# Kernel tuning notes

Measured on AMD Instinct MI355X. Metric: run time of the kernel, lower is better.

The kernel has to match this reference:

```python
import jax, jax.numpy as jnp
import numpy as np

DIM = 512
HEADS = 8
DIM_HEAD = 64
INNER = HEADS * DIM_HEAD  # 512
EPS = 1e-5


def _per_head_layernorm(t, gamma, beta):
    # t: [b, h, n, k]; gamma/beta: [h, k] (distinct LayerNorm per head)
    mu = jnp.mean(t, axis=-1, keepdims=True)
    var = jnp.mean(jnp.square(t - mu), axis=-1, keepdims=True)
    t_hat = (t - mu) * jax.lax.rsqrt(var + EPS)
    return t_hat * gamma[None, :, None, :] + beta[None, :, None, :]


def setup_inputs() -> dict:
    key = jax.random.key(0)
    ks = jax.random.split(key, 6)
    x = jax.random.normal(ks[0], (4, 8192, DIM), dtype=jnp.float32)
    # xavier_normal_ with gain=1e-4 on to_qkv weight [3*inner, dim]
    std_qkv = 1e-4 * np.sqrt(2.0 / (3 * INNER + DIM))
    W_qkv = jax.random.normal(ks[1], (3 * INNER, DIM), dtype=jnp.float32) * std_qkv
    gamma_K = jnp.ones((HEADS, DIM_HEAD), dtype=jnp.float32)
    beta_K = jnp.zeros((HEADS, DIM_HEAD), dtype=jnp.float32)
    gamma_V = jnp.ones((HEADS, DIM_HEAD), dtype=jnp.float32)
    beta_V = jnp.zeros((HEADS, DIM_HEAD), dtype=jnp.float32)
    std_out = np.sqrt(1.0 / INNER)
    W_out = jax.random.uniform(ks[2], (DIM, INNER), dtype=jnp.float32, minval=-std_out, maxval=std_out)
    b_out = jax.random.uniform(ks[3], (DIM,), dtype=jnp.float32, minval=-std_out, maxval=std_out)
    return {"x": x, "W_qkv": W_qkv, "gamma_K": gamma_K, "beta_K": beta_K,
            "gamma_V": gamma_V, "beta_V": beta_V, "W_out": W_out, "b_out": b_out}


def reference(x, W_qkv, gamma_K, beta_K, gamma_V, beta_V, W_out, b_out):
    b, n, _ = x.shape
    qkv = jnp.einsum('bnd,ed->bne', x, W_qkv)  # [b, n, 3*inner]
    q, k, v = jnp.split(qkv, 3, axis=-1)

    def to_heads(t):  # [b, n, h*k] -> [b, h, n, k]
        return t.reshape(b, n, HEADS, DIM_HEAD).transpose(0, 2, 1, 3)

    q, k, v = to_heads(q), to_heads(k), to_heads(v)
    k = _per_head_layernorm(k, gamma_K, beta_K)
    v = _per_head_layernorm(v, gamma_V, beta_V)

    # Galerkin linear attention: (K^T V)/n then Q @ (.)  -> O(n * d^2)
    p_attn = jnp.einsum('bhnk,bhnv->bhkv', k, v) / n  # [b, h, k, k]
    out = jnp.einsum('bhnk,bhkv->bhnv', q, p_attn)    # [b, h, n, k]
    out = out.transpose(0, 2, 1, 3).reshape(b, n, INNER)
    return jnp.einsum('bne,de->bnd', out, W_out) + b_out
```

## Files before the change

### kernel.cpp

```cpp
#include <hip/hip_runtime.h>


typedef __attribute__((ext_vector_type(8))) short bf16x8;
typedef __attribute__((ext_vector_type(4))) float f32x4;
typedef __attribute__((ext_vector_type(4))) unsigned short u16x4;

__device__ __forceinline__ unsigned short f2bf(float f) {
  unsigned int u = __builtin_bit_cast(unsigned int, f);
  u += 0x7FFFu + ((u >> 16) & 1u);
  return (unsigned short)(u >> 16);
}

__device__ __forceinline__ f32x4 mfma16(bf16x8 a, bf16x8 b, f32x4 c) {
  return __builtin_amdgcn_mfma_f32_16x16x32_bf16(a, b, c, 0, 0, 0);
}

__device__ __forceinline__ void gload16(const void* g, void* l) {
  __builtin_amdgcn_global_load_lds(
      (const __attribute__((address_space(1))) void*)g,
      (__attribute__((address_space(3))) void*)l, 16, 0, 0);
}

__global__ void k_cvt_bf16(const float* __restrict__ src,
                           unsigned short* __restrict__ dst, int n4) {
  int i = blockIdx.x * blockDim.x + threadIdx.x;
  if (i < n4) {
    float4 v = ((const float4*)src)[i];
    u16x4 o;
    o[0] = f2bf(v.x); o[1] = f2bf(v.y); o[2] = f2bf(v.z); o[3] = f2bf(v.w);
    ((u16x4*)dst)[i] = o;
  }
}

__device__ __forceinline__ void stage_tile(const unsigned short* pa,
                                           const unsigned short* pb,
                                           unsigned short* As, unsigned short* Bs,
                                           int w) {
#pragma unroll
  for (int j = 0; j < 4; ++j) {
    gload16(pa + j * 8 * 512, As + w * 2048 + j * 512);
    gload16(pb + j * 8 * 512, Bs + w * 2048 + j * 512);
  }
}

__device__ __forceinline__ void compute_tile(const unsigned short* As,
                                             const unsigned short* Bs,
                                             int wr, int wc, int g, int c16,
                                             f32x4 acc[4][4]) {
#pragma unroll
  for (int ks = 0; ks < 2; ++ks) {
    const int kcol = (ks * 32 + g * 8) ^ ((c16 & 7) << 3);
    bf16x8 af[4], bfv[4];
#pragma unroll
    for (int mi = 0; mi < 4; ++mi)
      af[mi] = *(const bf16x8*)&As[(wr * 64 + mi * 16 + c16) * 64 + kcol];
#pragma unroll
    for (int ni = 0; ni < 4; ++ni)
      bfv[ni] = *(const bf16x8*)&Bs[(wc * 64 + ni * 16 + c16) * 64 + kcol];
#pragma unroll
    for (int mi = 0; mi < 4; ++mi)
#pragma unroll
      for (int ni = 0; ni < 4; ++ni)
        acc[mi][ni] = mfma16(af[mi], bfv[ni], acc[mi][ni]);
  }
}

__launch_bounds__(256)
__global__ void k1_kvp(const unsigned short* __restrict__ xb,
                       const unsigned short* __restrict__ wqkvb,
                       const float* __restrict__ gK, const float* __restrict__ bK,
                       const float* __restrict__ gV, const float* __restrict__ bV,
                       float* __restrict__ P) {
  __shared__ __align__(16) unsigned short As[2][8192];
  __shared__ __align__(16) unsigned short Bs[2][8192];
  const int rt = blockIdx.x, h = blockIdx.y;
  const int tid = (int)threadIdx.x;
  const int l = tid & 63, w = tid >> 6;
  const int wr = w >> 1, wc = w & 1;
  const int g = l >> 4, c16 = l & 15;
  const int row0 = rt * 128;
  const int swz = ((l & 7) ^ (l >> 3)) * 8;

  const unsigned short* gsA = xb + (row0 + w * 32 + (l >> 3)) * 512 + swz;
  const int bcol = (w < 2) ? (512 + h * 64 + w * 32) : (1024 + h * 64 + (w - 2) * 32);
  const unsigned short* gsB = wqkvb + (bcol + (l >> 3)) * 512 + swz;

  f32x4 acc[4][4] = {};
  stage_tile(gsA, gsB, As[0], Bs[0], w);
  __syncthreads();
  for (int kt = 0; kt < 7; ++kt) {
    stage_tile(gsA + (kt + 1) * 64, gsB + (kt + 1) * 64,
               As[(kt + 1) & 1], Bs[(kt + 1) & 1], w);
    compute_tile(As[kt & 1], Bs[kt & 1], wr, wc, g, c16, acc);
    __syncthreads();
  }
  compute_tile(As[1], Bs[1], wr, wc, g, c16, acc);

  const float* gamma = (wc == 0) ? gK : gV;
  const float* beta  = (wc == 0) ? bK : bV;
  float gm[4], bt[4];
#pragma unroll
  for (int ni = 0; ni < 4; ++ni) {
    gm[ni] = gamma[h * 64 + ni * 16 + c16];
    bt[ni] = beta[h * 64 + ni * 16 + c16];
  }

  unsigned short* Kl = &As[0][0];
  unsigned short* Vl = &Bs[0][0];
  unsigned short* dst = (wc == 0) ? Kl : Vl;

#pragma unroll
  for (int mi = 0; mi < 4; ++mi) {
    float mean4[4], rs4[4];
#pragma unroll
    for (int r = 0; r < 4; ++r) {
      float a0 = acc[mi][0][r], a1 = acc[mi][1][r];
      float a2 = acc[mi][2][r], a3 = acc[mi][3][r];
      float s1 = a0 + a1 + a2 + a3;
      float s2 = a0 * a0 + a1 * a1 + a2 * a2 + a3 * a3;
#pragma unroll
      for (int m = 1; m <= 8; m <<= 1) {
        s1 += __shfl_xor(s1, m, 64);
        s2 += __shfl_xor(s2, m, 64);
      }
      const float mean = s1 * (1.0f / 64.0f);
      const float var = s2 * (1.0f / 64.0f) - mean * mean;
      mean4[r] = mean;
      rs4[r] = rsqrtf(var + 1e-5f);
    }
    const int n0 = wr * 64 + mi * 16 + g * 4;
#pragma unroll
    for (int ni = 0; ni < 4; ++ni) {
      const int d = ni * 16 + c16;
      u16x4 o;
#pragma unroll
      for (int r = 0; r < 4; ++r)
        o[r] = f2bf((acc[mi][ni][r] - mean4[r]) * rs4[r] * gm[ni] + bt[ni]);
      *(u16x4*)&dst[d * 128 + (((n0 >> 3) ^ c16) << 3) + (n0 & 7)] = o;
    }
  }
  __syncthreads();

  f32x4 pacc[4] = {};
#pragma unroll
  for (int ks = 0; ks < 4; ++ks) {
    const int p8 = (ks * 4 + g);
    bf16x8 af = *(const bf16x8*)&Kl[(w * 16 + c16) * 128 + ((p8 ^ c16) << 3)];
#pragma unroll
    for (int ni = 0; ni < 4; ++ni) {
      bf16x8 bfv = *(const bf16x8*)&Vl[(ni * 16 + c16) * 128 + ((p8 ^ c16) << 3)];
      pacc[ni] = mfma16(af, bfv, pacc[ni]);
    }
  }
  const int bh = (row0 >> 13) * 8 + h;
  float* Pp = P + bh * 4096;
#pragma unroll
  for (int ni = 0; ni < 4; ++ni)
#pragma unroll
    for (int r = 0; r < 4; ++r)
      atomicAdd(&Pp[(w * 16 + g * 4 + r) * 64 + ni * 16 + c16], pacc[ni][r]);
}

__launch_bounds__(256)
__global__ void k3a_g(const float* __restrict__ Wqkv,
                      const float* __restrict__ P,
                      unsigned short* __restrict__ Gt) {
  __shared__ float Pl[64 * 64];
  const int bh = blockIdx.x, dd = blockIdx.y;
  const int b = bh >> 3, h = bh & 7;
  const int t = (int)threadIdx.x;
  for (int i = t; i < 1024; i += 256)
    ((float4*)Pl)[i] = ((const float4*)(P + bh * 4096))[i];
  __syncthreads();

  const int qg = t >> 6, dl = t & 63;
  const int d = dd * 64 + dl;
  float acc[16] = {};
  for (int dh = 0; dh < 64; ++dh) {
    const float wq = Wqkv[(h * 64 + dh) * 512 + d];
    const float* pr = &Pl[dh * 64 + qg * 16];
#pragma unroll
    for (int i = 0; i < 16; ++i) acc[i] += pr[i] * wq;
  }
  unsigned short* go = &Gt[(b * 512 + d) * 512 + h * 64 + qg * 16];
#pragma unroll
  for (int i = 0; i < 16; ++i) go[i] = f2bf(acc[i] * (1.0f / 8192.0f));
}

__launch_bounds__(256)
__global__ void k3b_m(const unsigned short* __restrict__ wob,
                      const unsigned short* __restrict__ Gt,
                      unsigned short* __restrict__ Mb) {
  __shared__ __align__(16) unsigned short As[2][8192];
  __shared__ __align__(16) unsigned short Bs[2][8192];
  const int rt = blockIdx.x, ct = blockIdx.y, b = blockIdx.z;
  const int tid = (int)threadIdx.x;
  const int l = tid & 63, w = tid >> 6;
  const int wr = w >> 1, wc = w & 1;
  const int g = l >> 4, c16 = l & 15;
  const int row0 = rt * 128, col0 = ct * 128;
  const int swz = ((l & 7) ^ (l >> 3)) * 8;

  const unsigned short* gsA = wob + (row0 + w * 32 + (l >> 3)) * 512 + swz;
  const unsigned short* gsB = Gt + b * 262144 + (col0 + w * 32 + (l >> 3)) * 512 + swz;

  f32x4 acc[4][4] = {};
  stage_tile(gsA, gsB, As[0], Bs[0], w);
  __syncthreads();
  for (int kt = 0; kt < 7; ++kt) {
    stage_tile(gsA + (kt + 1) * 64, gsB + (kt + 1) * 64,
               As[(kt + 1) & 1], Bs[(kt + 1) & 1], w);
    compute_tile(As[kt & 1], Bs[kt & 1], wr, wc, g, c16, acc);
    __syncthreads();
  }
  compute_tile(As[1], Bs[1], wr, wc, g, c16, acc);

#pragma unroll
  for (int mi = 0; mi < 4; ++mi)
#pragma unroll
    for (int ni = 0; ni < 4; ++ni) {
      const int colg = col0 + wc * 64 + ni * 16 + c16;
#pragma unroll
      for (int r = 0; r < 4; ++r) {
        const int rowg = row0 + wr * 64 + mi * 16 + g * 4 + r;
        Mb[(b * 512 + rowg) * 512 + colg] = f2bf(acc[mi][ni][r]);
      }
    }
}

__launch_bounds__(256)
__global__ void k4_final(const unsigned short* __restrict__ xb,
                         const unsigned short* __restrict__ Mb,
                         const float* __restrict__ bout,
                         float* __restrict__ y) {
  __shared__ __align__(16) unsigned short As[2][8192];
  __shared__ __align__(16) unsigned short Bs[2][8192];
  const int rt = blockIdx.x, ct = blockIdx.y;
  const int tid = (int)threadIdx.x;
  const int l = tid & 63, w = tid >> 6;
  const int wr = w >> 1, wc = w & 1;
  const int g = l >> 4, c16 = l & 15;
  const int row0 = rt * 128, col0 = ct * 128;
  const int bb = row0 >> 13;
  const int swz = ((l & 7) ^ (l >> 3)) * 8;

  const unsigned short* gsA = xb + (row0 + w * 32 + (l >> 3)) * 512 + swz;
  const unsigned short* gsB = Mb + bb * 262144 + (col0 + w * 32 + (l >> 3)) * 512 + swz;

  f32x4 acc[4][4] = {};
  stage_tile(gsA, gsB, As[0], Bs[0], w);
  __syncthreads();
  for (int kt = 0; kt < 7; ++kt) {
    stage_tile(gsA + (kt + 1) * 64, gsB + (kt + 1) * 64,
               As[(kt + 1) & 1], Bs[(kt + 1) & 1], w);
    compute_tile(As[kt & 1], Bs[kt & 1], wr, wc, g, c16, acc);
    __syncthreads();
  }
  compute_tile(As[1], Bs[1], wr, wc, g, c16, acc);

  float bo[4];
#pragma unroll
  for (int ni = 0; ni < 4; ++ni)
    bo[ni] = bout[col0 + wc * 64 + ni * 16 + c16];
#pragma unroll
  for (int mi = 0; mi < 4; ++mi)
#pragma unroll
    for (int ni = 0; ni < 4; ++ni) {
      const int colg = col0 + wc * 64 + ni * 16 + c16;
#pragma unroll
      for (int r = 0; r < 4; ++r) {
        const int rowg = row0 + wr * 64 + mi * 16 + g * 4 + r;
        y[rowg * 512 + colg] = acc[mi][ni][r] + bo[ni];
      }
    }
}

extern "C" void kernel_launch(void* const* d_in, const int* in_sizes, int n_in,
                              void* d_out, int out_size, void* d_ws, size_t ws_size,
                              hipStream_t stream) {
  (void)in_sizes; (void)n_in; (void)out_size; (void)ws_size;
  const float* x    = (const float*)d_in[0];
  const float* Wqkv = (const float*)d_in[1];
  const float* gK   = (const float*)d_in[2];
  const float* bK   = (const float*)d_in[3];
  const float* gV   = (const float*)d_in[4];
  const float* bV   = (const float*)d_in[5];
  const float* Wout = (const float*)d_in[6];
  const float* bout = (const float*)d_in[7];
  float* y = (float*)d_out;

  char* w = (char*)d_ws;
  unsigned short* xb  = (unsigned short*)(w);
  unsigned short* Wb  = (unsigned short*)(w + 33554432);
  unsigned short* Wob = (unsigned short*)(w + 35127296);
  float*          P   = (float*)         (w + 35651584);
  unsigned short* Gt  = (unsigned short*)(w + 36175872);
  unsigned short* Mb  = (unsigned short*)(w + 38273024);

  k_cvt_bf16<<<16384, 256, 0, stream>>>(x, xb, 4194304);
  k_cvt_bf16<<<768, 256, 0, stream>>>(Wqkv, Wb, 196608);
  k_cvt_bf16<<<256, 256, 0, stream>>>(Wout, Wob, 65536);
  hipMemsetAsync(P, 0, 524288, stream);

  k1_kvp<<<dim3(256, 8), 256, 0, stream>>>(xb, Wb, gK, bK, gV, bV, P);
  k3a_g<<<dim3(32, 8), 256, 0, stream>>>(Wqkv, P, Gt);
  k3b_m<<<dim3(4, 4, 4), 256, 0, stream>>>(Wob, Gt, Mb);
  k4_final<<<dim3(256, 4), 256, 0, stream>>>(xb, Mb, bout, y);
}
```

Before: 145.9 us.

## Replace atomics with partial-sum buffer, single-buffer LDS, remap blocks across XCDs

The K/V-projection kernel now writes per-row-tile partial K^T V products to a workspace buffer, and a new reduction kernel sums them. This replaces the fp32 atomicAdd accumulation and the memset. All three GEMM kernels drop LDS double-buffering for a single buffer with two barriers per k-step. This halves LDS use, which may raise occupancy, but it loses the overlap between loads and compute. k1 and k4 also remap block IDs so neighbouring tiles land on the same XCD, aiming for better L2 locality. The cost is an extra 32 MB partial-buffer write and read plus one more kernel launch.

```diff
diff --git a/kernel.cpp b/kernel.cpp
--- a/kernel.cpp
+++ b/kernel.cpp
@@ -70,10 +70,12 @@
                        const unsigned short* __restrict__ wqkvb,
                        const float* __restrict__ gK, const float* __restrict__ bK,
                        const float* __restrict__ gV, const float* __restrict__ bV,
-                       float* __restrict__ P) {
-  __shared__ __align__(16) unsigned short As[2][8192];
-  __shared__ __align__(16) unsigned short Bs[2][8192];
-  const int rt = blockIdx.x, h = blockIdx.y;
+                       float* __restrict__ Ppart) {
+  __shared__ __align__(16) unsigned short As[8192];
+  __shared__ __align__(16) unsigned short Bs[8192];
+  const int bid = (int)blockIdx.x;
+  const int wgid = (bid & 7) * 256 + (bid >> 3);
+  const int rt = wgid >> 3, h = wgid & 7;
   const int tid = (int)threadIdx.x;
   const int l = tid & 63, w = tid >> 6;
   const int wr = w >> 1, wc = w & 1;
@@ -86,15 +88,12 @@
   const unsigned short* gsB = wqkvb + (bcol + (l >> 3)) * 512 + swz;
 
   f32x4 acc[4][4] = {};
-  stage_tile(gsA, gsB, As[0], Bs[0], w);
-  __syncthreads();
-  for (int kt = 0; kt < 7; ++kt) {
-    stage_tile(gsA + (kt + 1) * 64, gsB + (kt + 1) * 64,
-               As[(kt + 1) & 1], Bs[(kt + 1) & 1], w);
-    compute_tile(As[kt & 1], Bs[kt & 1], wr, wc, g, c16, acc);
-    __syncthreads();
-  }
-  compute_tile(As[1], Bs[1], wr, wc, g, c16, acc);
+  for (int kt = 0; kt < 8; ++kt) {
+    stage_tile(gsA + kt * 64, gsB + kt * 64, As, Bs, w);
+    __syncthreads();
+    compute_tile(As, Bs, wr, wc, g, c16, acc);
+    __syncthreads();
+  }
 
   const float* gamma = (wc == 0) ? gK : gV;
   const float* beta  = (wc == 0) ? bK : bV;
@@ -105,10 +104,7 @@
     bt[ni] = beta[h * 64 + ni * 16 + c16];
   }
 
-  unsigned short* Kl = &As[0][0];
-  unsigned short* Vl = &Bs[0][0];
-  unsigned short* dst = (wc == 0) ? Kl : Vl;
-
+  unsigned short* dst = (wc == 0) ? As : Bs;
 #pragma unroll
   for (int mi = 0; mi < 4; ++mi) {
     float mean4[4], rs4[4];
@@ -131,12 +127,11 @@
     const int n0 = wr * 64 + mi * 16 + g * 4;
 #pragma unroll
     for (int ni = 0; ni < 4; ++ni) {
-      const int d = ni * 16 + c16;
       u16x4 o;
 #pragma unroll
       for (int r = 0; r < 4; ++r)
         o[r] = f2bf((acc[mi][ni][r] - mean4[r]) * rs4[r] * gm[ni] + bt[ni]);
-      *(u16x4*)&dst[d * 128 + (((n0 >> 3) ^ c16) << 3) + (n0 & 7)] = o;
+      *(u16x4*)&dst[(ni * 16 + c16) * 128 + (((n0 >> 3) ^ c16) << 3) + (n0 & 7)] = o;
     }
   }
   __syncthreads();
@@ -144,21 +139,33 @@
   f32x4 pacc[4] = {};
 #pragma unroll
   for (int ks = 0; ks < 4; ++ks) {
-    const int p8 = (ks * 4 + g);
-    bf16x8 af = *(const bf16x8*)&Kl[(w * 16 + c16) * 128 + ((p8 ^ c16) << 3)];
+    const int grp = ((ks * 4 + g) ^ c16) << 3;
+    bf16x8 af = *(const bf16x8*)&As[(w * 16 + c16) * 128 + grp];
 #pragma unroll
     for (int ni = 0; ni < 4; ++ni) {
-      bf16x8 bfv = *(const bf16x8*)&Vl[(ni * 16 + c16) * 128 + ((p8 ^ c16) << 3)];
-      pacc[ni] = mfma16(af, bfv, pacc[ni]);
-    }
-  }
-  const int bh = (row0 >> 13) * 8 + h;
-  float* Pp = P + bh * 4096;
+      bf16x8 bv = *(const bf16x8*)&Bs[(ni * 16 + c16) * 128 + grp];
+      pacc[ni] = mfma16(af, bv, pacc[ni]);
+    }
+  }
+  const int bh = (rt >> 6) * 8 + h;
+  float* Pp = Ppart + ((size_t)(bh * 64 + (rt & 63))) * 4096;
 #pragma unroll
   for (int ni = 0; ni < 4; ++ni)
 #pragma unroll
     for (int r = 0; r < 4; ++r)
-      atomicAdd(&Pp[(w * 16 + g * 4 + r) * 64 + ni * 16 + c16], pacc[ni][r]);
+      Pp[(w * 16 + g * 4 + r) * 64 + ni * 16 + c16] = pacc[ni][r];
+}
+
+__launch_bounds__(256)
+__global__ void k_preduce(const float* __restrict__ Ppart,
+                          float* __restrict__ P) {
+  const int bh = blockIdx.x;
+  const int e = blockIdx.y * 256 + threadIdx.x;
+  const float* src = Ppart + (size_t)bh * 64 * 4096 + e;
+  float s = 0.f;
+#pragma unroll 8
+  for (int sl = 0; sl < 64; ++sl) s += src[sl * 4096];
+  P[bh * 4096 + e] = s;
 }
 
 __launch_bounds__(256)
@@ -191,8 +198,8 @@
 __global__ void k3b_m(const unsigned short* __restrict__ wob,
                       const unsigned short* __restrict__ Gt,
                       unsigned short* __restrict__ Mb) {
-  __shared__ __align__(16) unsigned short As[2][8192];
-  __shared__ __align__(16) unsigned short Bs[2][8192];
+  __shared__ __align__(16) unsigned short As[8192];
+  __shared__ __align__(16) unsigned short Bs[8192];
   const int rt = blockIdx.x, ct = blockIdx.y, b = blockIdx.z;
   const int tid = (int)threadIdx.x;
   const int l = tid & 63, w = tid >> 6;
@@ -205,15 +212,12 @@
   const unsigned short* gsB = Gt + b * 262144 + (col0 + w * 32 + (l >> 3)) * 512 + swz;
 
   f32x4 acc[4][4] = {};
-  stage_tile(gsA, gsB, As[0], Bs[0], w);
-  __syncthreads();
-  for (int kt = 0; kt < 7; ++kt) {
-    stage_tile(gsA + (kt + 1) * 64, gsB + (kt + 1) * 64,
-               As[(kt + 1) & 1], Bs[(kt + 1) & 1], w);
-    compute_tile(As[kt & 1], Bs[kt & 1], wr, wc, g, c16, acc);
-    __syncthreads();
-  }
-  compute_tile(As[1], Bs[1], wr, wc, g, c16, acc);
+  for (int kt = 0; kt < 8; ++kt) {
+    stage_tile(gsA + kt * 64, gsB + kt * 64, As, Bs, w);
+    __syncthreads();
+    compute_tile(As, Bs, wr, wc, g, c16, acc);
+    __syncthreads();
+  }
 
 #pragma unroll
   for (int mi = 0; mi < 4; ++mi)
@@ -233,9 +237,11 @@
                          const unsigned short* __restrict__ Mb,
                          const float* __restrict__ bout,
                          float* __restrict__ y) {
-  __shared__ __align__(16) unsigned short As[2][8192];
-  __shared__ __align__(16) unsigned short Bs[2][8192];
-  const int rt = blockIdx.x, ct = blockIdx.y;
+  __shared__ __align__(16) unsigned short As[8192];
+  __shared__ __align__(16) unsigned short Bs[8192];
+  const int bid = (int)blockIdx.x;
+  const int wgid = (bid & 7) * 128 + (bid >> 3);
+  const int rt = wgid >> 2, ct = wgid & 3;
   const int tid = (int)threadIdx.x;
   const int l = tid & 63, w = tid >> 6;
   const int wr = w >> 1, wc = w & 1;
@@ -248,15 +254,12 @@
   const unsigned short* gsB = Mb + bb * 262144 + (col0 + w * 32 + (l >> 3)) * 512 + swz;
 
   f32x4 acc[4][4] = {};
-  stage_tile(gsA, gsB, As[0], Bs[0], w);
-  __syncthreads();
-  for (int kt = 0; kt < 7; ++kt) {
-    stage_tile(gsA + (kt + 1) * 64, gsB + (kt + 1) * 64,
-               As[(kt + 1) & 1], Bs[(kt + 1) & 1], w);
-    compute_tile(As[kt & 1], Bs[kt & 1], wr, wc, g, c16, acc);
-    __syncthreads();
-  }
-  compute_tile(As[1], Bs[1], wr, wc, g, c16, acc);
+  for (int kt = 0; kt < 8; ++kt) {
+    stage_tile(gsA + kt * 64, gsB + kt * 64, As, Bs, w);
+    __syncthreads();
+    compute_tile(As, Bs, wr, wc, g, c16, acc);
+    __syncthreads();
+  }
 
   float bo[4];
 #pragma unroll
@@ -290,20 +293,21 @@
   float* y = (float*)d_out;
 
   char* w = (char*)d_ws;
-  unsigned short* xb  = (unsigned short*)(w);
-  unsigned short* Wb  = (unsigned short*)(w + 33554432);
-  unsigned short* Wob = (unsigned short*)(w + 35127296);
-  float*          P   = (float*)         (w + 35651584);
-  unsigned short* Gt  = (unsigned short*)(w + 36175872);
-  unsigned short* Mb  = (unsigned short*)(w + 38273024);
+  unsigned short* xb    = (unsigned short*)(w);
+  unsigned short* Wb    = (unsigned short*)(w + 33554432);
+  unsigned short* Wob   = (unsigned short*)(w + 35127296);
+  float*          P     = (float*)         (w + 35651584);
+  unsigned short* Gt    = (unsigned short*)(w + 36175872);
+  unsigned short* Mb    = (unsigned short*)(w + 38273024);
+  float*          Ppart = (float*)         (w + 40370176);
 
   k_cvt_bf16<<<16384, 256, 0, stream>>>(x, xb, 4194304);
   k_cvt_bf16<<<768, 256, 0, stream>>>(Wqkv, Wb, 196608);
   k_cvt_bf16<<<256, 256, 0, stream>>>(Wout, Wob, 65536);
-  hipMemsetAsync(P, 0, 524288, stream);
-
-  k1_kvp<<<dim3(256, 8), 256, 0, stream>>>(xb, Wb, gK, bK, gV, bV, P);
+
+  k1_kvp<<<2048, 256, 0, stream>>>(xb, Wb, gK, bK, gV, bV, Ppart);
+  k_preduce<<<dim3(32, 16), 256, 0, stream>>>(Ppart, P);
   k3a_g<<<dim3(32, 8), 256, 0, stream>>>(Wqkv, P, Gt);
   k3b_m<<<dim3(4, 4, 4), 256, 0, stream>>>(Wob, Gt, Mb);
-  k4_final<<<dim3(256, 4), 256, 0, stream>>>(xb, Mb, bout, y);
-}
+  k4_final<<<1024, 256, 0, stream>>>(xb, Mb, bout, y);
+}
```

New measurement: 133.6 us. 1.09x faster.
